# Kernel optimization log

Measured on AMD Instinct MI355X. Metric: run time of the kernel, lower is better.

Reference implementation:

```python
import jax, jax.numpy as jnp
import numpy as np

N_NODES = 100000
N_EDGES = 3200000
F_IN, F_HID, F_OUT = 36, 8, 2
NEG_SLOPE = 0.2


def gat_layer(x, src, dst, W, a_src, a_dst, b, num_nodes):
    # Linear transform: [N, F'] 
    h = x @ W
    # Per-node attention logits (heads=1)
    alpha_s = h @ a_src  # [N]
    alpha_d = h @ a_dst  # [N]
    # Edge-wise score: leaky_relu(a_src . h_j + a_dst . h_i) for edge j->i
    e = jax.nn.leaky_relu(alpha_s[src] + alpha_d[dst], negative_slope=NEG_SLOPE)  # [E]
    # Segment softmax over incoming edges of each dst node
    m = jax.ops.segment_max(e, dst, num_segments=num_nodes)  # [N]
    ee = jnp.exp(e - m[dst])
    denom = jax.ops.segment_sum(ee, dst, num_segments=num_nodes)  # [N]
    alpha = ee / denom[dst]  # [E]
    # Scatter-aggregate messages
    out = jax.ops.segment_sum(alpha[:, None] * h[src], dst, num_segments=num_nodes)
    return out + b


def setup_inputs() -> dict:
    key = jax.random.key(0)
    ks = jax.random.split(key, 10)
    x = jax.random.normal(ks[0], (N_NODES, F_IN), dtype=jnp.float32)
    edge_index = jax.random.randint(ks[1], (2, N_EDGES), 0, N_NODES, dtype=jnp.int64)
    s1 = 1.0 / np.sqrt(F_IN)
    s2 = 1.0 / np.sqrt(F_HID)
    W1 = jax.random.uniform(ks[2], (F_IN, F_HID), jnp.float32, -s1, s1)
    a_src1 = jax.random.uniform(ks[3], (F_HID,), jnp.float32, -s2, s2)
    a_dst1 = jax.random.uniform(ks[4], (F_HID,), jnp.float32, -s2, s2)
    b1 = jnp.zeros((F_HID,), jnp.float32)
    W2 = jax.random.uniform(ks[5], (F_HID, F_OUT), jnp.float32, -s2, s2)
    so = 1.0 / np.sqrt(F_OUT)
    a_src2 = jax.random.uniform(ks[6], (F_OUT,), jnp.float32, -so, so)
    a_dst2 = jax.random.uniform(ks[7], (F_OUT,), jnp.float32, -so, so)
    b2 = jnp.zeros((F_OUT,), jnp.float32)
    return {"x": x, "edge_index": edge_index, "W1": W1, "a_src1": a_src1,
            "a_dst1": a_dst1, "b1": b1, "W2": W2, "a_src2": a_src2,
            "a_dst2": a_dst2, "b2": b2}


def reference(x, edge_index, W1, a_src1, a_dst1, b1, W2, a_src2, a_dst2, b2):
    src, dst = edge_index[0], edge_index[1]
    n = x.shape[0]
    h = jax.nn.relu(gat_layer(x, src, dst, W1, a_src1, a_dst1, b1, n))
    # dropout is identity in eval mode
    out = gat_layer(h, src, dst, W2, a_src2, a_dst2, b2, n)
    return jax.nn.log_softmax(out, axis=1)
```

## Files before the change

kernel.cpp:

```cpp
#include <hip/hip_runtime.h>
#include <hip/hip_bf16.h>

#define N_NODES 100000
#define N_EDGES 3200000
#define F_IN 36
#define F_HID 8
#define F_OUT 2
#define NEG_SLOPE 0.2f

#define SHIFT 8
#define NPB 256
#define NBUCK 391
#define NB_PART 256
#define CHUNK 12500
#define NS (NBUCK * NB_PART)
#define BP 1024
#define ECAP 8704

__device__ __forceinline__ int detect_is64(const void* eidx, int* s_flag) {
    if (threadIdx.x < 64) {
        const unsigned int* p = (const unsigned int*)eidx;
        unsigned int v1 = p[2 * threadIdx.x + 1];
        unsigned int v2 = p[2 * (threadIdx.x + 64) + 1];
        unsigned long long m = __ballot(v1 != 0u || v2 != 0u);
        if (threadIdx.x == 0) *s_flag = (m == 0ull) ? 1 : 0;
    }
    __syncthreads();
    return *s_flag;
}

__global__ void count_k(const void* __restrict__ eidx, int* __restrict__ blk_cnt) {
    __shared__ int h[NBUCK];
    __shared__ int s_flag;
    int t = threadIdx.x;
    for (int i = t; i < NBUCK; i += BP) h[i] = 0;
    int f = detect_is64(eidx, &s_flag);
    __syncthreads();
    int beg = blockIdx.x * CHUNK;
    int end = beg + CHUNK; if (end > N_EDGES) end = N_EDGES;
    if (f) {
        const long long* p = (const long long*)eidx;
        for (int i = beg + t; i < end; i += BP) atomicAdd(&h[(int)p[N_EDGES + i] >> SHIFT], 1);
    } else {
        const int* p = (const int*)eidx;
        for (int i = beg + t; i < end; i += BP) atomicAdd(&h[p[N_EDGES + i] >> SHIFT], 1);
    }
    __syncthreads();
    for (int i = t; i < NBUCK; i += BP) blk_cnt[i * NB_PART + blockIdx.x] = h[i];
}

__global__ void scanA_k(int* __restrict__ blk_cnt, int* __restrict__ tot) {
    __shared__ int s[NB_PART];
    int t = threadIdx.x;
    int idx = blockIdx.x * NB_PART + t;
    int v = blk_cnt[idx];
    s[t] = v;
    __syncthreads();
    for (int o = 1; o < NB_PART; o <<= 1) {
        int u = (t >= o) ? s[t - o] : 0;
        __syncthreads();
        s[t] += u;
        __syncthreads();
    }
    blk_cnt[idx] = s[t] - v;
    if (t == NB_PART - 1) tot[blockIdx.x] = s[t];
}

__global__ void scanB_k(const int* __restrict__ tot, int* __restrict__ base) {
    __shared__ int s[512];
    int t = threadIdx.x;
    int orig = (t < NBUCK) ? tot[t] : 0;
    s[t] = orig;
    __syncthreads();
    for (int o = 1; o < 512; o <<= 1) {
        int u = (t >= o) ? s[t - o] : 0;
        __syncthreads();
        s[t] += u;
        __syncthreads();
    }
    if (t < NBUCK) base[t] = s[t] - orig;
    if (t == NBUCK - 1) base[NBUCK] = s[t];
}

__global__ void partition_k(const void* __restrict__ eidx, const int* __restrict__ blk_cnt,
                            const int* __restrict__ base, int* __restrict__ partP) {
    __shared__ int cur[NBUCK];
    __shared__ int s_flag;
    int t = threadIdx.x;
    int f = detect_is64(eidx, &s_flag);
    for (int i = t; i < NBUCK; i += BP)
        cur[i] = base[i] + blk_cnt[i * NB_PART + blockIdx.x];
    __syncthreads();
    int beg = blockIdx.x * CHUNK;
    int end = beg + CHUNK; if (end > N_EDGES) end = N_EDGES;
    if (f) {
        const long long* p = (const long long*)eidx;
        for (int i = beg + t; i < end; i += BP) {
            int s = (int)p[i];
            int d = (int)p[N_EDGES + i];
            int pos = atomicAdd(&cur[d >> SHIFT], 1);
            partP[pos] = (s << SHIFT) | (d & (NPB - 1));
        }
    } else {
        const int* p = (const int*)eidx;
        for (int i = beg + t; i < end; i += BP) {
            int s = p[i];
            int d = p[N_EDGES + i];
            int pos = atomicAdd(&cur[d >> SHIFT], 1);
            partP[pos] = (s << SHIFT) | (d & (NPB - 1));
        }
    }
}

__global__ void node1_k(const float* __restrict__ x, const float* __restrict__ W1,
                        const float* __restrict__ aw_s, const float* __restrict__ aw_d,
                        float* __restrict__ h1, float* __restrict__ as1, float* __restrict__ ad1,
                        int n_nodes) {
    int n = blockIdx.x * blockDim.x + threadIdx.x;
    if (n >= n_nodes) return;
    float acc[F_HID];
#pragma unroll
    for (int f = 0; f < F_HID; f++) acc[f] = 0.f;
    const float* xp = x + (size_t)n * F_IN;
#pragma unroll
    for (int k = 0; k < F_IN; k++) {
        float xv = xp[k];
#pragma unroll
        for (int f = 0; f < F_HID; f++) acc[f] += xv * W1[k * F_HID + f];
    }
    float s = 0.f, d = 0.f;
#pragma unroll
    for (int f = 0; f < F_HID; f++) {
        s += acc[f] * aw_s[f];
        d += acc[f] * aw_d[f];
        h1[(size_t)n * F_HID + f] = acc[f];
    }
    as1[n] = s;
    ad1[n] = d;
}

__global__ void gatF1_k(const int* __restrict__ base, const int* __restrict__ partP,
                        int* __restrict__ e_src, int* __restrict__ row_ptr,
                        const float* __restrict__ as1, const float* __restrict__ ad1,
                        const float* __restrict__ h1, const float* __restrict__ b1,
                        const float* __restrict__ W2, const float* __restrict__ aw_s2,
                        const float* __restrict__ aw_d2, float* __restrict__ h2,
                        float* __restrict__ as2, float* __restrict__ ad2) {
    __shared__ int eL[ECAP];
    __shared__ int hist[NPB];
    __shared__ int nstart[NPB];
    __shared__ int cursor[NPB];
    __shared__ int sscan[NPB];
    __shared__ float adl[NPB];
    int t = threadIdx.x;
    int b = blockIdx.x;
    int nbase = b << SHIFT;
    int beg = base[b], end = base[b + 1];
    int cnt = end - beg;
    int cap = cnt < ECAP ? cnt : ECAP;

    if (t < NPB) {
        hist[t] = 0;
        adl[t] = (nbase + t < N_NODES) ? ad1[nbase + t] : 0.f;
    }
    __syncthreads();
    for (int j = beg + t; j < end; j += BP)
        atomicAdd(&hist[partP[j] & (NPB - 1)], 1);
    __syncthreads();
    if (t < NPB) sscan[t] = hist[t];
    __syncthreads();
    for (int o = 1; o < NPB; o <<= 1) {
        int u = (t < NPB && t >= o) ? sscan[t - o] : 0;
        __syncthreads();
        if (t < NPB) sscan[t] += u;
        __syncthreads();
    }
    if (t < NPB) {
        int ex = sscan[t] - hist[t];
        nstart[t] = ex;
        cursor[t] = ex;
        int node = nbase + t;
        if (node < N_NODES) row_ptr[node] = beg + ex;
    }
    if (b == NBUCK - 1 && t == 0) row_ptr[N_NODES] = N_EDGES;
    __syncthreads();
    for (int j = beg + t; j < end; j += BP) {
        int pk = partP[j];
        int pos = atomicAdd(&cursor[pk & (NPB - 1)], 1);
        if (pos < ECAP) eL[pos] = pk >> SHIFT;
    }
    __syncthreads();
    for (int i = t; i < cap; i += BP) e_src[beg + i] = eL[i];

    int node = t >> 2;
    int lane = t & 3;
    int gnode = nbase + node;
    if (gnode >= N_NODES) return;
    int ns = nstart[node];
    int ne = ns + hist[node];
    if (ne > ECAP) ne = ECAP;
    float add = adl[node];

    float denom = 0.f;
    float acc[F_HID];
#pragma unroll
    for (int f = 0; f < F_HID; f++) acc[f] = 0.f;
    for (int i = ns + lane; i < ne; i += 4) {
        int s = eL[i];
        float e = as1[s] + add;
        e = e >= 0.f ? e : NEG_SLOPE * e;
        float ee = __expf(e);
        denom += ee;
        const float4* hp = (const float4*)(h1 + (size_t)s * F_HID);
        float4 p0 = hp[0], p1 = hp[1];
        acc[0] += ee * p0.x; acc[1] += ee * p0.y; acc[2] += ee * p0.z; acc[3] += ee * p0.w;
        acc[4] += ee * p1.x; acc[5] += ee * p1.y; acc[6] += ee * p1.z; acc[7] += ee * p1.w;
    }
#pragma unroll
    for (int o = 2; o > 0; o >>= 1) {
        denom += __shfl_xor(denom, o, 4);
#pragma unroll
        for (int f = 0; f < F_HID; f++) acc[f] += __shfl_xor(acc[f], o, 4);
    }
    if (lane == 0) {
        float inv = denom > 0.f ? 1.f / denom : 0.f;
        float o0 = 0.f, o1 = 0.f;
#pragma unroll
        for (int f = 0; f < F_HID; f++) {
            float v = acc[f] * inv + b1[f];
            v = v > 0.f ? v : 0.f;
            o0 += v * W2[f * F_OUT + 0];
            o1 += v * W2[f * F_OUT + 1];
        }
        ((float2*)h2)[gnode] = make_float2(o0, o1);
        as2[gnode] = o0 * aw_s2[0] + o1 * aw_s2[1];
        ad2[gnode] = o0 * aw_d2[0] + o1 * aw_d2[1];
    }
}

__global__ void gat2_k(const int* __restrict__ row_ptr, const int* __restrict__ e_src,
                       const float* __restrict__ as2, const float* __restrict__ ad2,
                       const float* __restrict__ h2, const float* __restrict__ b2,
                       float* __restrict__ out, int n_nodes) {
    int gid = blockIdx.x * 16 + (threadIdx.x >> 4);
    int lane = threadIdx.x & 15;
    if (gid >= n_nodes) return;
    int beg = row_ptr[gid], end = row_ptr[gid + 1];
    float add = ad2[gid];

    float denom = 0.f, a0 = 0.f, a1 = 0.f;
    for (int j = beg + lane; j < end; j += 16) {
        int s = e_src[j];
        float e = as2[s] + add;
        e = e >= 0.f ? e : NEG_SLOPE * e;
        float ee = __expf(e);
        denom += ee;
        float2 p = ((const float2*)h2)[s];
        a0 += ee * p.x;
        a1 += ee * p.y;
    }
#pragma unroll
    for (int o = 8; o > 0; o >>= 1) {
        denom += __shfl_xor(denom, o, 16);
        a0 += __shfl_xor(a0, o, 16);
        a1 += __shfl_xor(a1, o, 16);
    }

    if (lane == 0) {
        float inv = denom > 0.f ? 1.f / denom : 0.f;
        float o0 = a0 * inv + b2[0];
        float o1 = a1 * inv + b2[1];
        float M = fmaxf(o0, o1);
        float l = M + logf(__expf(o0 - M) + __expf(o1 - M));
        ((float2*)out)[gid] = make_float2(o0 - l, o1 - l);
    }
}

extern "C" void kernel_launch(void* const* d_in, const int* in_sizes, int n_in,
                              void* d_out, int out_size, void* d_ws, size_t ws_size,
                              hipStream_t stream) {
    const float* x      = (const float*)d_in[0];
    const void*  eidx   = d_in[1];
    const float* W1     = (const float*)d_in[2];
    const float* a_src1 = (const float*)d_in[3];
    const float* a_dst1 = (const float*)d_in[4];
    const float* b1     = (const float*)d_in[5];
    const float* W2     = (const float*)d_in[6];
    const float* a_src2 = (const float*)d_in[7];
    const float* a_dst2 = (const float*)d_in[8];
    const float* b2     = (const float*)d_in[9];
    float* out = (float*)d_out;

    const size_t N = N_NODES, E = N_EDGES;

    int* wsi = (int*)d_ws;
    float* wsf = (float*)d_ws;
    size_t o = 0;
    int* partP   = wsi + o;     o += E;
    int* e_src   = wsi + o;     o += E;
    int* blk_cnt = wsi + o;     o += NS;
    int* tot     = wsi + o;     o += 448;
    int* base    = wsi + o;     o += 400;
    int* row_ptr = wsi + o;     o += N + 64;
    float* as1   = wsf + o;     o += N;
    float* ad1   = wsf + o;     o += N;
    float* h1    = wsf + o;     o += 8 * N;
    float* h2    = wsf + o;     o += 2 * N;
    float* as2   = wsf + o;     o += N;
    float* ad2   = wsf + o;     o += N;

    const int B = 256;
    const int gridN = (int)((N + B - 1) / B);
    const int gridG = (int)(N / 16);

    count_k<<<NB_PART, BP, 0, stream>>>(eidx, blk_cnt);
    scanA_k<<<NBUCK, NB_PART, 0, stream>>>(blk_cnt, tot);
    scanB_k<<<1, 512, 0, stream>>>(tot, base);
    partition_k<<<NB_PART, BP, 0, stream>>>(eidx, blk_cnt, base, partP);

    node1_k<<<gridN, B, 0, stream>>>(x, W1, a_src1, a_dst1, h1, as1, ad1, (int)N);
    gatF1_k<<<NBUCK, BP, 0, stream>>>(base, partP, e_src, row_ptr, as1, ad1, h1, b1,
                                      W2, a_src2, a_dst2, h2, as2, ad2);
    gat2_k<<<gridG, B, 0, stream>>>(row_ptr, e_src, as2, ad2, h2, b2, out, (int)N);
}
```

Measured before the change: 196.2 us.

## Split each 256-node bucket across two 128-node blocks in gatF1_k

gatF1_k now launches two 512-thread blocks per 256-node partition bucket, each handling half the nodes. Both halves read the whole bucket; edges for the other half are filtered out, and a ballot-based count of first-half edges gives the second half its global offset. The aim is more, smaller blocks with less shared memory each, for better occupancy and CU utilisation. The cost is that every bucket's partP is read twice, plus extra ballot and atomic work.

```diff
diff --git a/kernel.cpp b/kernel.cpp
--- a/kernel.cpp
+++ b/kernel.cpp
@@ -15,7 +15,12 @@
 #define CHUNK 12500
 #define NS (NBUCK * NB_PART)
 #define BP 1024
-#define ECAP 8704
+
+#define GSHIFT 7
+#define GNPB 128
+#define GNBUCK 782
+#define BPG 512
+#define ECAP 4608
 
 __device__ __forceinline__ int detect_is64(const void* eidx, int* s_flag) {
     if (threadIdx.x < 64) {
@@ -147,50 +152,65 @@
                         const float* __restrict__ aw_d2, float* __restrict__ h2,
                         float* __restrict__ as2, float* __restrict__ ad2) {
     __shared__ int eL[ECAP];
-    __shared__ int hist[NPB];
-    __shared__ int nstart[NPB];
-    __shared__ int cursor[NPB];
-    __shared__ int sscan[NPB];
-    __shared__ float adl[NPB];
-    int t = threadIdx.x;
-    int b = blockIdx.x;
-    int nbase = b << SHIFT;
-    int beg = base[b], end = base[b + 1];
-    int cnt = end - beg;
-    int cap = cnt < ECAP ? cnt : ECAP;
-
-    if (t < NPB) {
+    __shared__ int hist[GNPB];
+    __shared__ int nstart[GNPB];
+    __shared__ int cursor[GNPB];
+    __shared__ int sscan[GNPB];
+    __shared__ float adl[GNPB];
+    __shared__ int s_sum0;
+    int t = threadIdx.x;
+    int c = blockIdx.x;
+    int p = c >> 1;
+    int half = c & 1;
+    int nbase = c << GSHIFT;
+    int pbeg = base[p], pend = base[p + 1];
+
+    if (t == 0) s_sum0 = 0;
+    if (t < GNPB) {
         hist[t] = 0;
         adl[t] = (nbase + t < N_NODES) ? ad1[nbase + t] : 0.f;
     }
     __syncthreads();
-    for (int j = beg + t; j < end; j += BP)
-        atomicAdd(&hist[partP[j] & (NPB - 1)], 1);
-    __syncthreads();
-    if (t < NPB) sscan[t] = hist[t];
-    __syncthreads();
-    for (int o = 1; o < NPB; o <<= 1) {
-        int u = (t < NPB && t >= o) ? sscan[t - o] : 0;
-        __syncthreads();
-        if (t < NPB) sscan[t] += u;
-        __syncthreads();
-    }
-    if (t < NPB) {
+    int niter = (pend - pbeg + BPG - 1) / BPG;
+    for (int it = 0; it < niter; it++) {
+        int j = pbeg + it * BPG + t;
+        bool inr = j < pend;
+        int pk = inr ? partP[j] : 0;
+        int hb = (pk >> GSHIFT) & 1;
+        unsigned long long mb = __ballot(inr && hb == 0);
+        if ((t & 63) == 0) atomicAdd(&s_sum0, (int)__popcll(mb));
+        if (inr && hb == half) atomicAdd(&hist[pk & (GNPB - 1)], 1);
+    }
+    __syncthreads();
+    if (t < GNPB) sscan[t] = hist[t];
+    __syncthreads();
+    for (int o = 1; o < GNPB; o <<= 1) {
+        int u = (t < GNPB && t >= o) ? sscan[t - o] : 0;
+        __syncthreads();
+        if (t < GNPB) sscan[t] += u;
+        __syncthreads();
+    }
+    int cbeg = pbeg + (half ? s_sum0 : 0);
+    if (t < GNPB) {
         int ex = sscan[t] - hist[t];
         nstart[t] = ex;
         cursor[t] = ex;
         int node = nbase + t;
-        if (node < N_NODES) row_ptr[node] = beg + ex;
-    }
-    if (b == NBUCK - 1 && t == 0) row_ptr[N_NODES] = N_EDGES;
-    __syncthreads();
-    for (int j = beg + t; j < end; j += BP) {
+        if (node < N_NODES) row_ptr[node] = cbeg + ex;
+    }
+    if (c == GNBUCK - 1 && t == 0) row_ptr[N_NODES] = N_EDGES;
+    __syncthreads();
+    for (int j = pbeg + t; j < pend; j += BPG) {
         int pk = partP[j];
-        int pos = atomicAdd(&cursor[pk & (NPB - 1)], 1);
-        if (pos < ECAP) eL[pos] = pk >> SHIFT;
-    }
-    __syncthreads();
-    for (int i = t; i < cap; i += BP) e_src[beg + i] = eL[i];
+        if (((pk >> GSHIFT) & 1) == half) {
+            int pos = atomicAdd(&cursor[pk & (GNPB - 1)], 1);
+            if (pos < ECAP) eL[pos] = pk >> SHIFT;
+        }
+    }
+    __syncthreads();
+    int cnt = sscan[GNPB - 1];
+    int cap = cnt < ECAP ? cnt : ECAP;
+    for (int i = t; i < cap; i += BPG) e_src[cbeg + i] = eL[i];
 
     int node = t >> 2;
     int lane = t & 3;
@@ -319,7 +339,7 @@
     partition_k<<<NB_PART, BP, 0, stream>>>(eidx, blk_cnt, base, partP);
 
     node1_k<<<gridN, B, 0, stream>>>(x, W1, a_src1, a_dst1, h1, as1, ad1, (int)N);
-    gatF1_k<<<NBUCK, BP, 0, stream>>>(base, partP, e_src, row_ptr, as1, ad1, h1, b1,
-                                      W2, a_src2, a_dst2, h2, as2, ad2);
+    gatF1_k<<<GNBUCK, BPG, 0, stream>>>(base, partP, e_src, row_ptr, as1, ad1, h1, b1,
+                                        W2, a_src2, a_dst2, h2, as2, ad2);
     gat2_k<<<gridG, B, 0, stream>>>(row_ptr, e_src, as2, ad2, h2, b2, out, (int)N);
 }
```

After: 200.7 us. +2.3%, slower.
